# Performance work log

Measured on AMD Instinct MI355X. Metric: run time of the kernel, lower is better.

Reference implementation:

```python
import jax, jax.numpy as jnp
import numpy as np

D = 512       # input_dim
K = 8         # output_size (number of bilinear slices)
L = 64        # hash_length
Q = 4096      # number of query vectors
C = 4096      # number of class vectors


def setup_inputs() -> dict:
    key = jax.random.key(0)
    ks = jax.random.split(key, 8)
    class_vector = jax.random.normal(ks[0], (C, D), dtype=jnp.float32)
    query_vector = jax.random.normal(ks[1], (Q, D), dtype=jnp.float32)
    # xavier_normal over (D, D, K): std = sqrt(2 / (fan_in + fan_out))
    xav = float(np.sqrt(2.0 / (D + D)))
    M = jax.random.normal(ks[2], (D, D, K), dtype=jnp.float32) * xav
    # score_layer: Linear(K, 1)
    lim_s = 1.0 / np.sqrt(K)
    score_w = jax.random.uniform(ks[3], (K,), jnp.float32, -lim_s, lim_s)
    score_b = jax.random.uniform(ks[4], (1,), jnp.float32, -lim_s, lim_s)
    # hash_layer: Linear(D, L) + Tanh
    lim_h = 1.0 / np.sqrt(D)
    hash_w = jax.random.uniform(ks[5], (L, D), jnp.float32, -lim_h, lim_h)
    hash_b = jax.random.uniform(ks[6], (L,), jnp.float32, -lim_h, lim_h)
    return {
        "class_vector": class_vector,
        "query_vector": query_vector,
        "M": M,
        "score_w": score_w,
        "score_b": score_b,
        "hash_w": hash_w,
        "hash_b": hash_b,
    }


def reference(class_vector, query_vector, M, score_w, score_b, hash_w, hash_b):
    # Looped bilinear product fused into one einsum:
    # inter_k = Q @ (C @ M[:,:,k]).T  ->  [Q, C, K]
    bi = jnp.einsum('ci,ijk,qj->qck', class_vector, M, query_vector)
    act = jax.nn.relu(bi)
    # score_layer: Linear(K, 1) then squeeze -> [Q, C]
    other = jnp.einsum('qck,k->qc', act, score_w) + score_b[0]
    relation_scores = jax.nn.softmax(other, axis=1)       # softmax over class dim
    query_features = relation_scores @ class_vector + query_vector  # [Q, D]
    hash_codes = jnp.tanh(query_features @ hash_w.T + hash_b)       # [Q, L]
    return hash_codes
```

## Files before the change

kernel.cpp:

```cpp
#include <hip/hip_runtime.h>
#include <hip/hip_bf16.h>
#include <math.h>

#define D_ 512
#define K_ 8
#define L_ 64
#define Q_ 4096
#define C_ 4096
#define N_ (C_ * K_)

typedef short short8 __attribute__((ext_vector_type(8)));
typedef float f32x4 __attribute__((ext_vector_type(4)));

static __device__ __forceinline__ void split2(float v, unsigned short& h, unsigned short& l) {
    __hip_bfloat16 hh = __float2bfloat16(v);
    float r = v - __bfloat162float(hh);
    __hip_bfloat16 ll = __float2bfloat16(r);
    h = *reinterpret_cast<unsigned short*>(&hh);
    l = *reinterpret_cast<unsigned short*>(&ll);
}

#define ASYNC_COPY16(gp, lp)                                                        \
    __builtin_amdgcn_global_load_lds((const __attribute__((address_space(1))) void*)(gp), \
                                     (__attribute__((address_space(3))) void*)(lp), \
                                     16, 0, 0)

__global__ void fused_prep(const float* __restrict__ M,
                           const float* __restrict__ class_v,
                           const float* __restrict__ query_v,
                           unsigned short* __restrict__ Mh, unsigned short* __restrict__ Ml,
                           unsigned short* __restrict__ Chh, unsigned short* __restrict__ Cll,
                           unsigned short* __restrict__ Qh, unsigned short* __restrict__ Ql) {
    __shared__ float t[64 * 65];
    const int b = blockIdx.x;
    const int tid = threadIdx.x;
    if (b < 512) {
        const int t0 = (b & 63) * 64;
        const int i0 = (b >> 6) * 64;
#pragma unroll
        for (int it = 0; it < 16; ++it) {
            int idx = tid + it * 256;
            int ri = idx >> 6, tc = idx & 63;
            t[tc * 65 + ri] = M[(size_t)(i0 + ri) * 4096 + t0 + tc];
        }
        __syncthreads();
        const int j0 = t0 >> 3;
#pragma unroll
        for (int it = 0; it < 16; ++it) {
            int odx = tid + it * 256;
            int tl = odx >> 6, ic = odx & 63;
            int n2 = (tl & 7) * 512 + j0 + (tl >> 3);
            size_t o = (size_t)n2 * 512 + i0 + ic;
            split2(t[tl * 65 + ic], Mh[o], Ml[o]);
        }
    } else if (b < 2560) {
        int i4 = ((b - 512) * 256 + tid) * 4;
        float4 v = *(const float4*)&class_v[i4];
        ushort4 h, l;
        split2(v.x, h.x, l.x);
        split2(v.y, h.y, l.y);
        split2(v.z, h.z, l.z);
        split2(v.w, h.w, l.w);
        *(ushort4*)&Chh[i4] = h;
        *(ushort4*)&Cll[i4] = l;
    } else {
        int i4 = ((b - 2560) * 256 + tid) * 4;
        float4 v = *(const float4*)&query_v[i4];
        ushort4 h, l;
        split2(v.x, h.x, l.x);
        split2(v.y, h.y, l.y);
        split2(v.z, h.z, l.z);
        split2(v.w, h.w, l.w);
        *(ushort4*)&Qh[i4] = h;
        *(ushort4*)&Ql[i4] = l;
    }
}

#define BM1 128
#define BN1 128
#define BNW1 32
#define BKK1 32

__device__ __forceinline__ void mfma_core_nt(
    const unsigned short* __restrict__ Agh, const unsigned short* __restrict__ Agl,
    const unsigned short* __restrict__ Bgh, const unsigned short* __restrict__ Bgl,
    int lda, int ldb, int kd, int m0, int n0,
    unsigned short (*Ahb)[BM1 * BKK1], unsigned short (*Alb)[BM1 * BKK1],
    f32x4 acc[8][2]) {
    const int tid = threadIdx.x;
    const int lane = tid & 63;
    const int wid = tid >> 6;
    const int fr = lane & 15;
    const int fq = lane >> 4;
    const int co = (fq ^ ((fr >> 1) & 3)) * 8;

    const unsigned short* ph0 = Bgh + (size_t)(n0 + wid * BNW1 + fr) * ldb + fq * 8;
    const unsigned short* ph1 = ph0 + 16 * (size_t)ldb;
    const unsigned short* pl0 = Bgl + (size_t)(n0 + wid * BNW1 + fr) * ldb + fq * 8;
    const unsigned short* pl1 = pl0 + 16 * (size_t)ldb;

    short8 bh[2][2], bl[2][2];

#define STAGE_A(k0_, buf_)                                                      \
    {                                                                           \
        _Pragma("unroll")                                                       \
        for (int h = 0; h < 2; ++h) {                                           \
            const int i2 = h * 256 + tid;                                       \
            const int r = i2 >> 2;                                              \
            const int cg = (i2 & 3) ^ ((r >> 1) & 3);                           \
            const int ldsoff = (h * 256 + (tid & ~63)) * 8;                     \
            const size_t go = (size_t)(m0 + r) * lda + (k0_) + cg * 8;          \
            ASYNC_COPY16(Agh + go, &Ahb[buf_][ldsoff]);                         \
            ASYNC_COPY16(Agl + go, &Alb[buf_][ldsoff]);                         \
        }                                                                       \
    }
#define LOAD_B_ASM(k0_, g_)                                                               \
    asm volatile("global_load_dwordx4 %0, %1, off" : "=v"(bh[g_][0]) : "v"(ph0 + (k0_))); \
    asm volatile("global_load_dwordx4 %0, %1, off" : "=v"(bh[g_][1]) : "v"(ph1 + (k0_))); \
    asm volatile("global_load_dwordx4 %0, %1, off" : "=v"(bl[g_][0]) : "v"(pl0 + (k0_))); \
    asm volatile("global_load_dwordx4 %0, %1, off" : "=v"(bl[g_][1]) : "v"(pl1 + (k0_)));

    const int niter = kd / BKK1;

    STAGE_A(0, 0)
    asm volatile("" ::: "memory");
    LOAD_B_ASM(0, 0)
    asm volatile("s_waitcnt vmcnt(4)" ::: "memory");
    __builtin_amdgcn_sched_barrier(0);
    asm volatile("s_barrier" ::: "memory");

#pragma unroll
    for (int it = 0; it < niter; ++it) {
        const int cur = it & 1, nxt = cur ^ 1;
        if (it + 1 < niter) {
            STAGE_A((it + 1) * BKK1, nxt)
        }
        asm volatile("" ::: "memory");
        if (it + 1 < niter) {
            LOAD_B_ASM((it + 1) * BKK1, nxt)
        }
        if (it + 1 < niter) {
            asm volatile("s_waitcnt vmcnt(8)" ::: "memory");
        } else {
            asm volatile("s_waitcnt vmcnt(0)" ::: "memory");
        }
        __builtin_amdgcn_sched_barrier(0);
#pragma unroll
        for (int mi = 0; mi < 8; ++mi) {
            const short8 ah = *(const short8*)&Ahb[cur][(mi * 16 + fr) * BKK1 + co];
            const short8 al = *(const short8*)&Alb[cur][(mi * 16 + fr) * BKK1 + co];
#pragma unroll
            for (int ni = 0; ni < 2; ++ni)
                acc[mi][ni] = __builtin_amdgcn_mfma_f32_16x16x32_bf16(ah, bh[cur][ni], acc[mi][ni], 0, 0, 0);
#pragma unroll
            for (int ni = 0; ni < 2; ++ni)
                acc[mi][ni] = __builtin_amdgcn_mfma_f32_16x16x32_bf16(ah, bl[cur][ni], acc[mi][ni], 0, 0, 0);
#pragma unroll
            for (int ni = 0; ni < 2; ++ni)
                acc[mi][ni] = __builtin_amdgcn_mfma_f32_16x16x32_bf16(al, bh[cur][ni], acc[mi][ni], 0, 0, 0);
        }
        if (it + 1 < niter) {
            asm volatile("s_waitcnt vmcnt(4)" ::: "memory");
            __builtin_amdgcn_sched_barrier(0);
            asm volatile("s_barrier" ::: "memory");
        }
    }
#undef STAGE_A
#undef LOAD_B_ASM
}

__launch_bounds__(256, 4)
__global__ void bilinear_mfma(const unsigned short* __restrict__ Qh,
                              const unsigned short* __restrict__ Ql,
                              const unsigned short* __restrict__ Ph,
                              const unsigned short* __restrict__ Pl,
                              const float* __restrict__ sw,
                              const float* __restrict__ sb,
                              float* __restrict__ other) {
    __shared__ __attribute__((aligned(16))) unsigned short Ahb[2][BM1 * BKK1];
    __shared__ __attribute__((aligned(16))) unsigned short Alb[2][BM1 * BKK1];
    const int tid = threadIdx.x;
    const int lane = tid & 63;
    const int wid = tid >> 6;
    const int fr = lane & 15;
    const int fq = lane >> 4;
    f32x4 acc[8][2] = {};
    const int q0 = blockIdx.x * BM1;
    const int n0 = blockIdx.y * BN1;
    mfma_core_nt(Qh, Ql, Ph, Pl, D_, D_, D_, q0, n0, Ahb, Alb, acc);
    const float wk = sw[lane & 7];
    const float bias = sb[0];
#pragma unroll
    for (int mi = 0; mi < 8; ++mi)
#pragma unroll
        for (int ni = 0; ni < 2; ++ni)
#pragma unroll
            for (int r = 0; r < 4; ++r) {
                float v2 = wk * fmaxf(acc[mi][ni][r], 0.f);
                v2 += __shfl_xor(v2, 1);
                v2 += __shfl_xor(v2, 2);
                v2 += __shfl_xor(v2, 4);
                if ((lane & 7) == 0) {
                    int q = q0 + mi * 16 + fq * 4 + r;
                    int c = (n0 + wid * BNW1 + ni * 16 + fr) >> 3;
                    other[(size_t)q * C_ + c] = v2 + bias;
                }
            }
}

#define OPS_ 8192
#define BUFS_ (4 * OPS_)

__device__ __forceinline__ void mfma_core8(
    const unsigned short* __restrict__ Agh, const unsigned short* __restrict__ Agl,
    const unsigned short* __restrict__ Bgh, const unsigned short* __restrict__ Bgl,
    const int lda, const int ldb, const int kd, const int m0, const int n0,
    unsigned short* Lds, f32x4 acc[8][4]) {
    const int tid = threadIdx.x;
    const int lane = tid & 63;
    const int wid = tid >> 6;
    const int fr = lane & 15;
    const int co = ((lane >> 4) ^ ((fr >> 1) & 3)) * 8;
    const int wm = (wid >> 2) * 128;
    const int wn = (wid & 3) * 64;
    const int nt = kd >> 5;
    const int aoff = (wm + fr) * 32 + co;
    const int boff = (wn + fr) * 32 + co;

#define STAGE8(k0_, buf_)                                                              \
    {                                                                                  \
        _Pragma("unroll")                                                              \
        for (int h_ = 0; h_ < 2; ++h_) {                                               \
            const int i2_ = h_ * 512 + tid;                                            \
            const int r_ = i2_ >> 2;                                                   \
            const int cg_ = (i2_ & 3) ^ ((r_ >> 1) & 3);                               \
            unsigned short* lp_ = Lds + (buf_) * BUFS_ + (h_ * 512 + (tid & ~63)) * 8; \
            const size_t ga_ = (size_t)(m0 + r_) * lda + (k0_) + cg_ * 8;              \
            const size_t gb_ = (size_t)(n0 + r_) * ldb + (k0_) + cg_ * 8;              \
            ASYNC_COPY16(Agh + ga_, lp_);                                              \
            ASYNC_COPY16(Agl + ga_, lp_ + OPS_);                                       \
            ASYNC_COPY16(Bgh + gb_, lp_ + 2 * OPS_);                                   \
            ASYNC_COPY16(Bgl + gb_, lp_ + 3 * OPS_);                                   \
        }                                                                              \
    }

#define QUAD(MH, NH)                                                                         \
    _Pragma("unroll")                                                                        \
    for (int i_ = 0; i_ < 4; ++i_) {                                                         \
        _Pragma("unroll")                                                                    \
        for (int j_ = 0; j_ < 2; ++j_) {                                                     \
            f32x4& a_ = acc[(MH) * 4 + i_][(NH) * 2 + j_];                                   \
            a_ = __builtin_amdgcn_mfma_f32_16x16x32_bf16(ah[i_], bhv[(NH) * 2 + j_], a_, 0, 0, 0); \
        }                                                                                    \
    }                                                                                        \
    _Pragma("unroll")                                                                        \
    for (int i_ = 0; i_ < 4; ++i_) {                                                         \
        _Pragma("unroll")                                                                    \
        for (int j_ = 0; j_ < 2; ++j_) {                                                     \
            f32x4& a_ = acc[(MH) * 4 + i_][(NH) * 2 + j_];                                   \
            a_ = __builtin_amdgcn_mfma_f32_16x16x32_bf16(ah[i_], blv[(NH) * 2 + j_], a_, 0, 0, 0); \
        }                                                                                    \
    }                                                                                        \
    _Pragma("unroll")                                                                        \
    for (int i_ = 0; i_ < 4; ++i_) {                                                         \
        _Pragma("unroll")                                                                    \
        for (int j_ = 0; j_ < 2; ++j_) {                                                     \
            f32x4& a_ = acc[(MH) * 4 + i_][(NH) * 2 + j_];                                   \
            a_ = __builtin_amdgcn_mfma_f32_16x16x32_bf16(al[i_], bhv[(NH) * 2 + j_], a_, 0, 0, 0); \
        }                                                                                    \
    }

    STAGE8(0, 0)
    STAGE8(32, 1)
    asm volatile("s_waitcnt vmcnt(8)" ::: "memory");
    __builtin_amdgcn_sched_barrier(0);
    __builtin_amdgcn_s_barrier();

#pragma unroll 2
    for (int t = 0; t < nt; ++t) {
        const int cur = t & 1;
        const unsigned short* Lc = Lds + cur * BUFS_;
        short8 ah[4], al[4], bhv[4], blv[4];

#pragma unroll
        for (int i = 0; i < 4; ++i) {
            ah[i] = *(const short8*)(Lc + aoff + i * 512);
            al[i] = *(const short8*)(Lc + OPS_ + aoff + i * 512);
        }
#pragma unroll
        for (int j = 0; j < 2; ++j) {
            bhv[j] = *(const short8*)(Lc + 2 * OPS_ + boff + j * 512);
            blv[j] = *(const short8*)(Lc + 3 * OPS_ + boff + j * 512);
        }
        __builtin_amdgcn_s_barrier();
        asm volatile("s_waitcnt lgkmcnt(0)" ::: "memory");
        __builtin_amdgcn_sched_barrier(0);
        __builtin_amdgcn_s_setprio(1);
        QUAD(0, 0)
        __builtin_amdgcn_s_setprio(0);
        __builtin_amdgcn_s_barrier();

#pragma unroll
        for (int j = 2; j < 4; ++j) {
            bhv[j] = *(const short8*)(Lc + 2 * OPS_ + boff + j * 512);
            blv[j] = *(const short8*)(Lc + 3 * OPS_ + boff + j * 512);
        }
        __builtin_amdgcn_s_barrier();
        asm volatile("s_waitcnt lgkmcnt(0)" ::: "memory");
        __builtin_amdgcn_sched_barrier(0);
        __builtin_amdgcn_s_setprio(1);
        QUAD(0, 1)
        __builtin_amdgcn_s_setprio(0);
        __builtin_amdgcn_s_barrier();

#pragma unroll
        for (int i = 0; i < 4; ++i) {
            ah[i] = *(const short8*)(Lc + aoff + 2048 + i * 512);
            al[i] = *(const short8*)(Lc + OPS_ + aoff + 2048 + i * 512);
        }
        __builtin_amdgcn_s_barrier();
        asm volatile("s_waitcnt lgkmcnt(0)" ::: "memory");
        __builtin_amdgcn_sched_barrier(0);
        __builtin_amdgcn_s_setprio(1);
        QUAD(1, 1)
        __builtin_amdgcn_s_setprio(0);
        __builtin_amdgcn_s_barrier();

        if (t + 2 < nt) STAGE8((t + 2) * 32, cur)
        __builtin_amdgcn_s_barrier();
        __builtin_amdgcn_s_setprio(1);
        QUAD(1, 0)
        __builtin_amdgcn_s_setprio(0);
        if (t + 2 < nt) {
            asm volatile("s_waitcnt vmcnt(8)" ::: "memory");
        } else if (t + 1 < nt) {
            asm volatile("s_waitcnt vmcnt(0)" ::: "memory");
        }
        __builtin_amdgcn_sched_barrier(0);
        __builtin_amdgcn_s_barrier();
    }
#undef STAGE8
#undef QUAD
}

__launch_bounds__(512, 2)
__global__ void gemm_P_mfma8(const unsigned short* __restrict__ Chh,
                             const unsigned short* __restrict__ Cll,
                             const unsigned short* __restrict__ Mh,
                             const unsigned short* __restrict__ Ml,
                             unsigned short* __restrict__ Ph,
                             unsigned short* __restrict__ Pl) {
    __shared__ __attribute__((aligned(16))) unsigned short Lds[2 * BUFS_];
    f32x4 acc[8][4] = {};
    const int n0 = blockIdx.x * 256;
    const int c0 = blockIdx.y * 256;
    mfma_core8(Chh, Cll, Mh, Ml, D_, D_, D_, c0, n0, Lds, acc);
    const int lane = threadIdx.x & 63;
    const int wid = threadIdx.x >> 6;
    const int fr = lane & 15, fq = lane >> 4;
    const int wm = (wid >> 2) * 128, wn = (wid & 3) * 64;
#pragma unroll
    for (int mi = 0; mi < 8; ++mi)
#pragma unroll
        for (int ni = 0; ni < 4; ++ni)
#pragma unroll
            for (int r = 0; r < 4; ++r) {
                int c = c0 + wm + mi * 16 + fq * 4 + r;
                int n2 = n0 + wn + ni * 16 + fr;
                size_t o = (size_t)c * (K_ * D_) + n2;
                split2(acc[mi][ni][r], Ph[o], Pl[o]);
            }
}

__launch_bounds__(512, 2)
__global__ void gemm_qf_mfma8(const unsigned short* __restrict__ Sh,
                              const unsigned short* __restrict__ Sl,
                              const unsigned short* __restrict__ Th,
                              const unsigned short* __restrict__ Tl,
                              float* __restrict__ qfp_base) {
    __shared__ __attribute__((aligned(16))) unsigned short Lds[2 * BUFS_];
    f32x4 acc[8][4] = {};
    const int n0 = blockIdx.x * 256;
    const int q0 = blockIdx.y * 256;
    const int zoff = blockIdx.z * (C_ / 8);
    float* qfp = qfp_base + (size_t)blockIdx.z * Q_ * D_;
    mfma_core8(Sh + zoff, Sl + zoff, Th + zoff, Tl + zoff,
               C_, C_, C_ / 8, q0, n0, Lds, acc);
    const int lane = threadIdx.x & 63;
    const int wid = threadIdx.x >> 6;
    const int fr = lane & 15, fq = lane >> 4;
    const int wm = (wid >> 2) * 128, wn = (wid & 3) * 64;
#pragma unroll
    for (int mi = 0; mi < 8; ++mi)
#pragma unroll
        for (int ni = 0; ni < 4; ++ni)
#pragma unroll
            for (int r = 0; r < 4; ++r) {
                int q = q0 + wm + mi * 16 + fq * 4 + r;
                int d = n0 + wn + ni * 16 + fr;
                qfp[(size_t)q * D_ + d] = acc[mi][ni][r];
            }
}

__launch_bounds__(256)
__global__ void fused_softmax_tc(const float* __restrict__ other,
                                 unsigned short* __restrict__ Sh,
                                 unsigned short* __restrict__ Sl,
                                 const float* __restrict__ class_v,
                                 unsigned short* __restrict__ Th,
                                 unsigned short* __restrict__ Tl) {
    __shared__ float smem[64 * 65];
    const int b = blockIdx.x;
    const int tid = threadIdx.x;
    if (b < 4096) {
        const int q = b;
        const float* row = other + (size_t)q * C_;
        float v[16];
        float m = -1e30f;
#pragma unroll
        for (int it = 0; it < 16; ++it) {
            v[it] = row[tid + it * 256];
            m = fmaxf(m, v[it]);
        }
#pragma unroll
        for (int off = 32; off; off >>= 1) m = fmaxf(m, __shfl_down(m, off));
        if ((tid & 63) == 0) smem[tid >> 6] = m;
        __syncthreads();
        m = fmaxf(fmaxf(smem[0], smem[1]), fmaxf(smem[2], smem[3]));
        __syncthreads();
        float s = 0.f;
#pragma unroll
        for (int it = 0; it < 16; ++it) {
            v[it] = __expf(v[it] - m);
            s += v[it];
        }
#pragma unroll
        for (int off = 32; off; off >>= 1) s += __shfl_down(s, off);
        if ((tid & 63) == 0) smem[tid >> 6] = s;
        __syncthreads();
        const float inv = 1.f / (smem[0] + smem[1] + smem[2] + smem[3]);
#pragma unroll
        for (int it = 0; it < 16; ++it) {
            size_t o = (size_t)q * C_ + tid + it * 256;
            split2(v[it] * inv, Sh[o], Sl[o]);
        }
    } else {
        const int bb = b - 4096;
        const int c0 = (bb & 63) * 64;
        const int d0 = (bb >> 6) * 64;
#pragma unroll
        for (int it = 0; it < 16; ++it) {
            int idx = tid + it * 256;
            int rc = idx >> 6, dc = idx & 63;
            smem[dc * 65 + rc] = class_v[(size_t)(c0 + rc) * 512 + d0 + dc];
        }
        __syncthreads();
#pragma unroll
        for (int it = 0; it < 16; ++it) {
            int odx = tid + it * 256;
            int dr = odx >> 6, cc = odx & 63;
            size_t o = (size_t)(d0 + dr) * 4096 + c0 + cc;
            split2(smem[dr * 65 + cc], Th[o], Tl[o]);
        }
    }
}

__launch_bounds__(256)
__global__ void hash_kernel(const float* __restrict__ qfp_base,
                            const float* __restrict__ Qv,
                            const float* __restrict__ hw,
                            const float* __restrict__ hb,
                            float* __restrict__ out) {
    __shared__ float sqf[4 * D_];
    const int q0 = blockIdx.x * 4;
    const int tid = threadIdx.x;
    {
        const float4* sq = (const float4*)&Qv[(size_t)q0 * D_];
        float4* dst = (float4*)sqf;
#pragma unroll
        for (int it = 0; it < 2; ++it) {
            int i = tid + it * 256;
            float4 o = sq[i];
#pragma unroll
            for (int z = 0; z < 8; ++z) {
                const float4 a =
                    ((const float4*)&qfp_base[(size_t)z * Q_ * D_ + (size_t)q0 * D_])[i];
                o.x += a.x; o.y += a.y; o.z += a.z; o.w += a.w;
            }
            dst[i] = o;
        }
    }
    __syncthreads();
    const int l = tid % L_;
    const int qi = tid / L_;
    float s = hb[l];
    const float* wrow = &hw[(size_t)l * D_];
    const float* xrow = &sqf[qi * D_];
#pragma unroll 4
    for (int d = 0; d < D_; d += 4) {
        float4 w4 = *(const float4*)&wrow[d];
        float4 x4 = *(const float4*)&xrow[d];
        s += x4.x * w4.x + x4.y * w4.y + x4.z * w4.z + x4.w * w4.w;
    }
    out[(size_t)(q0 + qi) * L_ + l] = tanhf(s);
}

extern "C" void kernel_launch(void* const* d_in, const int* in_sizes, int n_in,
                              void* d_out, int out_size, void* d_ws, size_t ws_size,
                              hipStream_t stream) {
    const float* class_v = (const float*)d_in[0];
    const float* query_v = (const float*)d_in[1];
    const float* M       = (const float*)d_in[2];
    const float* score_w = (const float*)d_in[3];
    const float* score_b = (const float*)d_in[4];
    const float* hash_w  = (const float*)d_in[5];
    const float* hash_b  = (const float*)d_in[6];
    float* out = (float*)d_out;

    char* base = (char*)d_ws;
    unsigned short* Ph = (unsigned short*)base;
    unsigned short* Pl = (unsigned short*)(base + (size_t)33554432);
    char* oreg          = base + (size_t)67108864;
    float* other        = (float*)oreg;
    unsigned short* Mh  = (unsigned short*)oreg;
    unsigned short* Ml  = (unsigned short*)(oreg + (size_t)4194304);
    unsigned short* Chh = (unsigned short*)(oreg + (size_t)8388608);
    unsigned short* Cll = (unsigned short*)(oreg + (size_t)12582912);
    float* qfp          = (float*)oreg;
    char* scratch = base + (size_t)134217728;
    unsigned short* Qh = (unsigned short*)scratch;
    unsigned short* Ql = (unsigned short*)(scratch + (size_t)4194304);
    unsigned short* Th = (unsigned short*)scratch;
    unsigned short* Tl = (unsigned short*)(scratch + (size_t)4194304);
    unsigned short* Sh = Ph;
    unsigned short* Sl = Pl;

    fused_prep<<<4608, 256, 0, stream>>>(M, class_v, query_v, Mh, Ml, Chh, Cll, Qh, Ql);
    gemm_P_mfma8<<<dim3((K_ * D_) / 256, C_ / 256), 512, 0, stream>>>(Chh, Cll, Mh, Ml, Ph, Pl);
    bilinear_mfma<<<dim3(Q_ / BM1, N_ / BN1), 256, 0, stream>>>(Qh, Ql, Ph, Pl,
                                                                score_w, score_b, other);
    fused_softmax_tc<<<4608, 256, 0, stream>>>(other, Sh, Sl, class_v, Th, Tl);
    gemm_qf_mfma8<<<dim3(D_ / 256, Q_ / 256, 8), 512, 0, stream>>>(Sh, Sl, Th, Tl, qfp);
    hash_kernel<<<Q_ / 4, 256, 0, stream>>>(qfp, query_v, hash_w, hash_b, out);
}
```

Baseline: 658.8 us.

## Precompute Q·M per slice and reduce bilinear over K inside the accumulator loop

The bilinear stage now multiplies Q by M first, giving G[q, k*512+j], instead of multiplying C by M. The second GEMM streams G as the A operand over a 4096-long reduction, split into 8 segments of 512. After each segment it applies ReLU and the score weight into a running sum, so each output element is written once without cross-lane shuffles. The B operand is small class data reloaded cyclically and likely stays cache-resident. In exchange, the main kernel has a long serial reduction and double accumulator registers at lower occupancy (launch bounds 2), and the explicit vmcnt waits now run on compiler-generated loads.

Result: slower. 696.1 us (+5.7%).

```diff
diff --git a/kernel.cpp b/kernel.cpp
--- a/kernel.cpp
+++ b/kernel.cpp
@@ -48,10 +48,11 @@
 #pragma unroll
         for (int it = 0; it < 16; ++it) {
             int odx = tid + it * 256;
-            int tl = odx >> 6, ic = odx & 63;
-            int n2 = (tl & 7) * 512 + j0 + (tl >> 3);
-            size_t o = (size_t)n2 * 512 + i0 + ic;
-            split2(t[tl * 65 + ic], Mh[o], Ml[o]);
+            int jl = odx & 7;
+            int il = (odx >> 3) & 63;
+            int k  = odx >> 9;
+            size_t o = (size_t)(k * 512 + i0 + il) * 512 + j0 + jl;
+            split2(t[(jl * 8 + k) * 65 + il], Mh[o], Ml[o]);
         }
     } else if (b < 2560) {
         int i4 = ((b - 512) * 256 + tid) * 4;
@@ -81,12 +82,16 @@
 #define BNW1 32
 #define BKK1 32
 
-__device__ __forceinline__ void mfma_core_nt(
-    const unsigned short* __restrict__ Agh, const unsigned short* __restrict__ Agl,
-    const unsigned short* __restrict__ Bgh, const unsigned short* __restrict__ Bgl,
-    int lda, int ldb, int kd, int m0, int n0,
-    unsigned short (*Ahb)[BM1 * BKK1], unsigned short (*Alb)[BM1 * BKK1],
-    f32x4 acc[8][2]) {
+__launch_bounds__(256, 2)
+__global__ void bilinear_seg(const unsigned short* __restrict__ Gh,
+                             const unsigned short* __restrict__ Gl,
+                             const unsigned short* __restrict__ Ch,
+                             const unsigned short* __restrict__ Cl,
+                             const float* __restrict__ sw,
+                             const float* __restrict__ sb,
+                             float* __restrict__ other) {
+    __shared__ __attribute__((aligned(16))) unsigned short Ahb[2][BM1 * BKK1];
+    __shared__ __attribute__((aligned(16))) unsigned short Alb[2][BM1 * BKK1];
     const int tid = threadIdx.x;
     const int lane = tid & 63;
     const int wid = tid >> 6;
@@ -94,12 +99,17 @@
     const int fq = lane >> 4;
     const int co = (fq ^ ((fr >> 1) & 3)) * 8;
 
-    const unsigned short* ph0 = Bgh + (size_t)(n0 + wid * BNW1 + fr) * ldb + fq * 8;
-    const unsigned short* ph1 = ph0 + 16 * (size_t)ldb;
-    const unsigned short* pl0 = Bgl + (size_t)(n0 + wid * BNW1 + fr) * ldb + fq * 8;
-    const unsigned short* pl1 = pl0 + 16 * (size_t)ldb;
+    const int c0 = blockIdx.x * BN1;
+    const int q0 = blockIdx.y * BM1;
+
+    const unsigned short* pbh0 = Ch + (size_t)(c0 + wid * BNW1 + fr) * D_ + fq * 8;
+    const unsigned short* pbh1 = pbh0 + 16 * (size_t)D_;
+    const unsigned short* pbl0 = Cl + (size_t)(c0 + wid * BNW1 + fr) * D_ + fq * 8;
+    const unsigned short* pbl1 = pbl0 + 16 * (size_t)D_;
 
     short8 bh[2][2], bl[2][2];
+    f32x4 acc[8][2] = {};
+    f32x4 sum[8][2] = {};
 
 #define STAGE_A(k0_, buf_)                                                      \
     {                                                                           \
@@ -109,42 +119,35 @@
             const int r = i2 >> 2;                                              \
             const int cg = (i2 & 3) ^ ((r >> 1) & 3);                           \
             const int ldsoff = (h * 256 + (tid & ~63)) * 8;                     \
-            const size_t go = (size_t)(m0 + r) * lda + (k0_) + cg * 8;          \
-            ASYNC_COPY16(Agh + go, &Ahb[buf_][ldsoff]);                         \
-            ASYNC_COPY16(Agl + go, &Alb[buf_][ldsoff]);                         \
+            const size_t go = (size_t)(q0 + r) * 4096 + (k0_) + cg * 8;         \
+            ASYNC_COPY16(Gh + go, &Ahb[buf_][ldsoff]);                          \
+            ASYNC_COPY16(Gl + go, &Alb[buf_][ldsoff]);                          \
         }                                                                       \
     }
-#define LOAD_B_ASM(k0_, g_)                                                               \
-    asm volatile("global_load_dwordx4 %0, %1, off" : "=v"(bh[g_][0]) : "v"(ph0 + (k0_))); \
-    asm volatile("global_load_dwordx4 %0, %1, off" : "=v"(bh[g_][1]) : "v"(ph1 + (k0_))); \
-    asm volatile("global_load_dwordx4 %0, %1, off" : "=v"(bl[g_][0]) : "v"(pl0 + (k0_))); \
-    asm volatile("global_load_dwordx4 %0, %1, off" : "=v"(bl[g_][1]) : "v"(pl1 + (k0_)));
-
-    const int niter = kd / BKK1;
+#define LOAD_B(j0_, g_)                                                         \
+    bh[g_][0] = *(const short8*)(pbh0 + (j0_));                                 \
+    bh[g_][1] = *(const short8*)(pbh1 + (j0_));                                 \
+    bl[g_][0] = *(const short8*)(pbl0 + (j0_));                                 \
+    bl[g_][1] = *(const short8*)(pbl1 + (j0_));
 
     STAGE_A(0, 0)
     asm volatile("" ::: "memory");
-    LOAD_B_ASM(0, 0)
+    LOAD_B(0, 0)
     asm volatile("s_waitcnt vmcnt(4)" ::: "memory");
     __builtin_amdgcn_sched_barrier(0);
     asm volatile("s_barrier" ::: "memory");
 
-#pragma unroll
-    for (int it = 0; it < niter; ++it) {
+#pragma unroll 2
+    for (int it = 0; it < 128; ++it) {
         const int cur = it & 1, nxt = cur ^ 1;
-        if (it + 1 < niter) {
+        if (it + 1 < 128) {
             STAGE_A((it + 1) * BKK1, nxt)
         }
         asm volatile("" ::: "memory");
-        if (it + 1 < niter) {
-            LOAD_B_ASM((it + 1) * BKK1, nxt)
-        }
-        if (it + 1 < niter) {
-            asm volatile("s_waitcnt vmcnt(8)" ::: "memory");
-        } else {
-            asm volatile("s_waitcnt vmcnt(0)" ::: "memory");
-        }
-        __builtin_amdgcn_sched_barrier(0);
+        if (it + 1 < 128) {
+            const int j0n = ((it + 1) & 15) * BKK1;
+            LOAD_B(j0n, nxt)
+        }
 #pragma unroll
         for (int mi = 0; mi < 8; ++mi) {
             const short8 ah = *(const short8*)&Ahb[cur][(mi * 16 + fr) * BKK1 + co];
@@ -159,36 +162,27 @@
             for (int ni = 0; ni < 2; ++ni)
                 acc[mi][ni] = __builtin_amdgcn_mfma_f32_16x16x32_bf16(al, bh[cur][ni], acc[mi][ni], 0, 0, 0);
         }
-        if (it + 1 < niter) {
+        if ((it & 15) == 15) {
+            const float swk = sw[it >> 4];
+#pragma unroll
+            for (int mi = 0; mi < 8; ++mi)
+#pragma unroll
+                for (int ni = 0; ni < 2; ++ni) {
+#pragma unroll
+                    for (int r = 0; r < 4; ++r)
+                        sum[mi][ni][r] += swk * fmaxf(acc[mi][ni][r], 0.f);
+                    acc[mi][ni] = (f32x4){0.f, 0.f, 0.f, 0.f};
+                }
+        }
+        if (it + 1 < 128) {
             asm volatile("s_waitcnt vmcnt(4)" ::: "memory");
             __builtin_amdgcn_sched_barrier(0);
             asm volatile("s_barrier" ::: "memory");
         }
     }
 #undef STAGE_A
-#undef LOAD_B_ASM
-}
-
-__launch_bounds__(256, 4)
-__global__ void bilinear_mfma(const unsigned short* __restrict__ Qh,
-                              const unsigned short* __restrict__ Ql,
-                              const unsigned short* __restrict__ Ph,
-                              const unsigned short* __restrict__ Pl,
-                              const float* __restrict__ sw,
-                              const float* __restrict__ sb,
-                              float* __restrict__ other) {
-    __shared__ __attribute__((aligned(16))) unsigned short Ahb[2][BM1 * BKK1];
-    __shared__ __attribute__((aligned(16))) unsigned short Alb[2][BM1 * BKK1];
-    const int tid = threadIdx.x;
-    const int lane = tid & 63;
-    const int wid = tid >> 6;
-    const int fr = lane & 15;
-    const int fq = lane >> 4;
-    f32x4 acc[8][2] = {};
-    const int q0 = blockIdx.x * BM1;
-    const int n0 = blockIdx.y * BN1;
-    mfma_core_nt(Qh, Ql, Ph, Pl, D_, D_, D_, q0, n0, Ahb, Alb, acc);
-    const float wk = sw[lane & 7];
+#undef LOAD_B
+
     const float bias = sb[0];
 #pragma unroll
     for (int mi = 0; mi < 8; ++mi)
@@ -196,15 +190,9 @@
         for (int ni = 0; ni < 2; ++ni)
 #pragma unroll
             for (int r = 0; r < 4; ++r) {
-                float v2 = wk * fmaxf(acc[mi][ni][r], 0.f);
-                v2 += __shfl_xor(v2, 1);
-                v2 += __shfl_xor(v2, 2);
-                v2 += __shfl_xor(v2, 4);
-                if ((lane & 7) == 0) {
-                    int q = q0 + mi * 16 + fq * 4 + r;
-                    int c = (n0 + wid * BNW1 + ni * 16 + fr) >> 3;
-                    other[(size_t)q * C_ + c] = v2 + bias;
-                }
+                int q = q0 + mi * 16 + fq * 4 + r;
+                int c = c0 + wid * BNW1 + ni * 16 + fr;
+                other[(size_t)q * C_ + c] = sum[mi][ni][r] + bias;
             }
 }
 
@@ -344,17 +332,17 @@
 }
 
 __launch_bounds__(512, 2)
-__global__ void gemm_P_mfma8(const unsigned short* __restrict__ Chh,
-                             const unsigned short* __restrict__ Cll,
+__global__ void gemm_G_mfma8(const unsigned short* __restrict__ Qh,
+                             const unsigned short* __restrict__ Ql,
                              const unsigned short* __restrict__ Mh,
                              const unsigned short* __restrict__ Ml,
-                             unsigned short* __restrict__ Ph,
-                             unsigned short* __restrict__ Pl) {
+                             unsigned short* __restrict__ Gh,
+                             unsigned short* __restrict__ Gl) {
     __shared__ __attribute__((aligned(16))) unsigned short Lds[2 * BUFS_];
     f32x4 acc[8][4] = {};
     const int n0 = blockIdx.x * 256;
-    const int c0 = blockIdx.y * 256;
-    mfma_core8(Chh, Cll, Mh, Ml, D_, D_, D_, c0, n0, Lds, acc);
+    const int q0 = blockIdx.y * 256;
+    mfma_core8(Qh, Ql, Mh, Ml, D_, D_, D_, q0, n0, Lds, acc);
     const int lane = threadIdx.x & 63;
     const int wid = threadIdx.x >> 6;
     const int fr = lane & 15, fq = lane >> 4;
@@ -365,10 +353,10 @@
         for (int ni = 0; ni < 4; ++ni)
 #pragma unroll
             for (int r = 0; r < 4; ++r) {
-                int c = c0 + wm + mi * 16 + fq * 4 + r;
+                int q = q0 + wm + mi * 16 + fq * 4 + r;
                 int n2 = n0 + wn + ni * 16 + fr;
-                size_t o = (size_t)c * (K_ * D_) + n2;
-                split2(acc[mi][ni][r], Ph[o], Pl[o]);
+                size_t o = (size_t)q * (K_ * D_) + n2;
+                split2(acc[mi][ni][r], Gh[o], Gl[o]);
             }
 }
 
@@ -518,27 +506,27 @@
     float* out = (float*)d_out;
 
     char* base = (char*)d_ws;
-    unsigned short* Ph = (unsigned short*)base;
-    unsigned short* Pl = (unsigned short*)(base + (size_t)33554432);
+    unsigned short* Gh = (unsigned short*)base;
+    unsigned short* Gl = (unsigned short*)(base + (size_t)33554432);
     char* oreg          = base + (size_t)67108864;
     float* other        = (float*)oreg;
     unsigned short* Mh  = (unsigned short*)oreg;
     unsigned short* Ml  = (unsigned short*)(oreg + (size_t)4194304);
-    unsigned short* Chh = (unsigned short*)(oreg + (size_t)8388608);
-    unsigned short* Cll = (unsigned short*)(oreg + (size_t)12582912);
+    unsigned short* Qh  = (unsigned short*)(oreg + (size_t)8388608);
+    unsigned short* Ql  = (unsigned short*)(oreg + (size_t)12582912);
     float* qfp          = (float*)oreg;
     char* scratch = base + (size_t)134217728;
-    unsigned short* Qh = (unsigned short*)scratch;
-    unsigned short* Ql = (unsigned short*)(scratch + (size_t)4194304);
-    unsigned short* Th = (unsigned short*)scratch;
-    unsigned short* Tl = (unsigned short*)(scratch + (size_t)4194304);
-    unsigned short* Sh = Ph;
-    unsigned short* Sl = Pl;
+    unsigned short* Chh = (unsigned short*)scratch;
+    unsigned short* Cll = (unsigned short*)(scratch + (size_t)4194304);
+    unsigned short* Th  = (unsigned short*)scratch;
+    unsigned short* Tl  = (unsigned short*)(scratch + (size_t)4194304);
+    unsigned short* Sh = Gh;
+    unsigned short* Sl = Gl;
 
     fused_prep<<<4608, 256, 0, stream>>>(M, class_v, query_v, Mh, Ml, Chh, Cll, Qh, Ql);
-    gemm_P_mfma8<<<dim3((K_ * D_) / 256, C_ / 256), 512, 0, stream>>>(Chh, Cll, Mh, Ml, Ph, Pl);
-    bilinear_mfma<<<dim3(Q_ / BM1, N_ / BN1), 256, 0, stream>>>(Qh, Ql, Ph, Pl,
-                                                                score_w, score_b, other);
+    gemm_G_mfma8<<<dim3((K_ * D_) / 256, Q_ / 256), 512, 0, stream>>>(Qh, Ql, Mh, Ml, Gh, Gl);
+    bilinear_seg<<<dim3(C_ / BN1, Q_ / BM1), 256, 0, stream>>>(Gh, Gl, Chh, Cll,
+                                                               score_w, score_b, other);
     fused_softmax_tc<<<4608, 256, 0, stream>>>(other, Sh, Sl, class_v, Th, Tl);
     gemm_qf_mfma8<<<dim3(D_ / 256, Q_ / 256, 8), 512, 0, stream>>>(Sh, Sl, Th, Tl, qfp);
     hash_kernel<<<Q_ / 4, 256, 0, stream>>>(qfp, query_v, hash_w, hash_b, out);
```
